# Kernel optimization log

Measured on AMD Instinct MI355X. Metric: run time of the kernel, lower is better.

## Reference

```python
import jax, jax.numpy as jnp
import numpy as np

E = 300000        # num_edges
T = 3000000       # num_triplets
D = 128           # edge_message_dim
N_RAD = 6
N_SPH = 7
D_DOWN = 64       # edge_down_dim
D_BAS = 8         # basis_embed_dim


def _w(key, fan_in, fan_out):
    return jax.random.normal(key, (fan_in, fan_out), jnp.float32) / np.sqrt(fan_in)


def setup_inputs() -> dict:
    key = jax.random.key(0)
    ks = jax.random.split(key, 32)
    inp = {
        "x": jax.random.normal(ks[0], (E, D), jnp.float32),
        "rbf": jax.random.uniform(ks[1], (E, N_RAD), jnp.float32),
        "sbf": jax.random.uniform(ks[2], (T, N_SPH * N_RAD), jnp.float32),
        "idx_kj": jax.random.randint(ks[3], (T,), 0, E),
        "idx_ji": jax.random.randint(ks[4], (T,), 0, E),
        # basis projections (bias-free)
        "w_rbf1": _w(ks[5], N_RAD, D_BAS),
        "w_rbf2": _w(ks[6], D_BAS, D),
        "w_sbf1": _w(ks[7], N_SPH * N_RAD, D_BAS),
        "w_sbf2": _w(ks[8], D_BAS, D_DOWN),
        # message linears (with bias)
        "w_kj": _w(ks[9], D, D), "b_kj": jnp.zeros((D,), jnp.float32),
        "w_ji": _w(ks[10], D, D), "b_ji": jnp.zeros((D,), jnp.float32),
        # down / up projections (bias-free)
        "w_down": _w(ks[11], D, D_DOWN),
        "w_up": _w(ks[12], D_DOWN, D),
        # residual block before skip + dense
        "res1_w1": _w(ks[13], D, D), "res1_b1": jnp.zeros((D,), jnp.float32),
        "res1_w2": _w(ks[14], D, D), "res1_b2": jnp.zeros((D,), jnp.float32),
        "w_bs": _w(ks[15], D, D), "b_bs": jnp.zeros((D,), jnp.float32),
        # two residual blocks after skip
        "res2_w1": _w(ks[16], D, D), "res2_b1": jnp.zeros((D,), jnp.float32),
        "res2_w2": _w(ks[17], D, D), "res2_b2": jnp.zeros((D,), jnp.float32),
        "res3_w1": _w(ks[18], D, D), "res3_b1": jnp.zeros((D,), jnp.float32),
        "res3_w2": _w(ks[19], D, D), "res3_b2": jnp.zeros((D,), jnp.float32),
    }
    return inp


def _res_block(h, w1, b1, w2, b2):
    # h + act(lin2(act(lin1(h)))) with Swish(beta=1) == silu
    return h + jax.nn.silu(jax.nn.silu(h @ w1 + b1) @ w2 + b2)


def reference(x, rbf, sbf, idx_kj, idx_ji,
              w_rbf1, w_rbf2, w_sbf1, w_sbf2,
              w_kj, b_kj, w_ji, b_ji, w_down, w_up,
              res1_w1, res1_b1, res1_w2, res1_b2, w_bs, b_bs,
              res2_w1, res2_b1, res2_w2, res2_b2,
              res3_w1, res3_b1, res3_w2, res3_b2):
    act = jax.nn.silu
    x_ji = act(x @ w_ji + b_ji)                       # [E, D]
    x_kj = act(x @ w_kj + b_kj)                       # [E, D]
    rbf_e = (rbf @ w_rbf1) @ w_rbf2                   # [E, D]
    x_kj = act((x_kj * rbf_e) @ w_down)               # [E, D_DOWN]
    sbf_e = (sbf @ w_sbf1) @ w_sbf2                   # [T, D_DOWN]
    m = x_kj[idx_kj] * sbf_e                          # gather + Hadamard [T, D_DOWN]
    agg = jax.ops.segment_sum(m, idx_ji, num_segments=x.shape[0])  # [E, D_DOWN]
    x_kj = act(agg @ w_up)                            # [E, D]
    h = _res_block(x_ji + x_kj, res1_w1, res1_b1, res1_w2, res1_b2)
    h = act(h @ w_bs + b_bs) + x                      # skip connection
    h = _res_block(h, res2_w1, res2_b1, res2_w2, res2_b2)
    h = _res_block(h, res3_w1, res3_b1, res3_w2, res3_b2)
    return h
```

## Files before the change

kernel.cpp:

```cpp
#include <hip/hip_runtime.h>
#include <hip/hip_bf16.h>


typedef __attribute__((ext_vector_type(8))) short bf16x8;
typedef __attribute__((ext_vector_type(4))) float f32x4;
typedef __attribute__((ext_vector_type(4))) unsigned int u32x4;

__device__ __forceinline__ float silu_f(float v) {
    return v * __builtin_amdgcn_rcpf(1.0f + __expf(-v));
}
__device__ __forceinline__ short f2bf(float f) {
    unsigned u = __float_as_uint(f);
    unsigned r = u + 0x7fffu + ((u >> 16) & 1u);
    return (short)(r >> 16);
}
__device__ __forceinline__ float bf2f(short s) {
    return __uint_as_float(((unsigned)(unsigned short)s) << 16);
}

__device__ __forceinline__ unsigned cvt_pk_bf16(float a, float b) {
    __hip_bfloat162 h = __float22bfloat162_rn(float2{a, b});
    return *reinterpret_cast<unsigned*>(&h);
}
__device__ __forceinline__ void split44(f32x4 a, f32x4 b, bf16x8& hi, bf16x8& lo) {
    float f[8] = {a[0], a[1], a[2], a[3], b[0], b[1], b[2], b[3]};
    u32x4 H, L;
    #pragma unroll
    for (int j = 0; j < 4; ++j) {
        const float f0 = f[2 * j], f1 = f[2 * j + 1];
        const unsigned h = cvt_pk_bf16(f0, f1);
        const float r0 = f0 - __uint_as_float(h << 16);
        const float r1 = f1 - __uint_as_float(h & 0xffff0000u);
        H[j] = h;
        L[j] = cvt_pk_bf16(r0, r1);
    }
    hi = __builtin_bit_cast(bf16x8, H);
    lo = __builtin_bit_cast(bf16x8, L);
}

__device__ __forceinline__ void gll16(const void* g, void* l) {
    __builtin_amdgcn_global_load_lds((const __attribute__((address_space(1))) void*)g,
                                     (__attribute__((address_space(3))) void*)l, 16, 0, 0);
}
__device__ __forceinline__ void stage16(const char* g, short* l, int lane, int wid) {
    #pragma unroll
    for (int i = 0; i < 4; ++i) {
        const int off = ((i * 4 + wid) << 10);
        gll16(g + off + lane * 16, (char*)l + off);
    }
}
__device__ __forceinline__ void stage8(const char* g, short* l, int lane, int wid) {
    #pragma unroll
    for (int i = 0; i < 2; ++i) {
        const int off = ((i * 4 + wid) << 10);
        gll16(g + off + lane * 16, (char*)l + off);
    }
}

template<int NF>
__device__ __forceinline__ void mfma_ks(bf16x8 ah, bf16x8 al, const short* slot,
                                        int acol, int kq, f32x4* acc) {
    #pragma unroll
    for (int n = 0; n < NF; ++n) {
        const int c = n * 16 + acol;
        const int x = (c >> 2) & 1;
        const int sw = (kq ^ (c & 3)) << 3;
        const bf16x8 bh = *(const bf16x8*)&slot[c * 64 + x * 32 + sw];
        const bf16x8 bl = *(const bf16x8*)&slot[c * 64 + (x ^ 1) * 32 + sw];
        acc[n] = __builtin_amdgcn_mfma_f32_16x16x32_bf16(ah, bh, acc[n], 0, 0, 0);
        acc[n] = __builtin_amdgcn_mfma_f32_16x16x32_bf16(al, bh, acc[n], 0, 0, 0);
        acc[n] = __builtin_amdgcn_mfma_f32_16x16x32_bf16(ah, bl, acc[n], 0, 0, 0);
    }
}
template<int NF>
__device__ __forceinline__ void gphase(f32x4 a0, f32x4 a1, const short* slot,
                                       int acol, int kq, f32x4* acc) {
    bf16x8 ah, al; split44(a0, a1, ah, al);
    mfma_ks<NF>(ah, al, slot, acol, kq, acc);
}
template<int NF>
__device__ __forceinline__ void tphase(const float* tl, int rowbase, int q,
                                       int kq, int acol, const short* slot, f32x4* acc) {
    const f32x4 ta = *(const f32x4*)&tl[rowbase + q * 32 + kq * 8];
    const f32x4 tb = *(const f32x4*)&tl[rowbase + q * 32 + kq * 8 + 4];
    bf16x8 ah, al; split44(ta, tb, ah, al);
    mfma_ks<NF>(ah, al, slot, acol, kq, acc);
}

__device__ __forceinline__ void tgemm4(const char* img, const char* imgnext,
                                       short* sA, short* sB, const float* tl, int rb,
                                       int kq, int acol, int lane, int wid, f32x4* acc)
{
    stage16(img + 16384, sB, lane, wid);
    tphase<8>(tl, rb, 0, kq, acol, sA, acc); __syncthreads();
    stage16(img + 32768, sA, lane, wid);
    tphase<8>(tl, rb, 1, kq, acol, sB, acc); __syncthreads();
    stage16(img + 49152, sB, lane, wid);
    tphase<8>(tl, rb, 2, kq, acol, sA, acc); __syncthreads();
    if (imgnext) stage16(imgnext, sA, lane, wid);
    tphase<8>(tl, rb, 3, kq, acol, sB, acc); __syncthreads();
}

#define TPITCH 132

struct WDesc { const float* src; char* dst; int K; int N; };
struct WPrepArgs { WDesc w[11]; };

__global__ void wprep_kernel(WPrepArgs args) {
    const WDesc d = args.w[blockIdx.y];
    const int h = blockIdx.x;
    if (h * 32 >= d.K) return;
    char* slab = d.dst + (size_t)h * d.N * 128;
    for (int idx = threadIdx.x; idx < d.N * 4; idx += 256) {
        const int c = idx >> 2, ch = idx & 3;
        bf16x8 hi, lo;
        #pragma unroll
        for (int j = 0; j < 8; ++j) {
            const float f = d.src[(size_t)(h * 32 + ch * 8 + j) * d.N + c];
            const short hb = f2bf(f);
            hi[j] = hb;
            lo[j] = f2bf(f - bf2f(hb));
        }
        const int x = (c >> 2) & 1;
        const int sw = (ch ^ (c & 3)) * 16;
        *(bf16x8*)(slab + c * 128 + x * 64 + sw)       = hi;
        *(bf16x8*)(slab + c * 128 + (x ^ 1) * 64 + sw) = lo;
    }
}


__global__ void rbf1_kernel(const float* __restrict__ rbf, const float* __restrict__ w_rbf1,
                            float* __restrict__ re1, int E) {
    const int i = blockIdx.x * 256 + threadIdx.x;
    const int e = i >> 3, p = i & 7;
    if (e < E) {
        float s = 0.f;
        #pragma unroll
        for (int q = 0; q < 6; ++q) s = fmaf(rbf[e * 6 + q], w_rbf1[q * 8 + p], s);
        re1[i] = s;
    }
}

__global__ void count_rank_kernel(const int* __restrict__ idx_ji, int* __restrict__ cnt,
                                  int* __restrict__ rank, int T) {
    const int i = (blockIdx.x * 256 + threadIdx.x) * 4;
    if (i + 3 < T) {
        const int4 j = *(const int4*)&idx_ji[i];
        int4 r;
        r.x = atomicAdd(&cnt[j.x], 1);
        r.y = atomicAdd(&cnt[j.y], 1);
        r.z = atomicAdd(&cnt[j.z], 1);
        r.w = atomicAdd(&cnt[j.w], 1);
        *(int4*)&rank[i] = r;
    } else {
        for (int k = i; k < T; ++k) rank[k] = atomicAdd(&cnt[idx_ji[k]], 1);
    }
}

__global__ void scan_partial_kernel(const int* __restrict__ cnt, int* __restrict__ partial, int E) {
    __shared__ int red[256];
    const int tid = threadIdx.x;
    const int base = blockIdx.x * 1024 + tid * 4;
    int s = 0;
    #pragma unroll
    for (int i = 0; i < 4; ++i) { const int g = base + i; if (g < E) s += cnt[g]; }
    red[tid] = s;
    __syncthreads();
    for (int off = 128; off > 0; off >>= 1) {
        if (tid < off) red[tid] += red[tid + off];
        __syncthreads();
    }
    if (tid == 0) partial[blockIdx.x] = red[0];
}

__global__ void scan_block_kernel(const int* __restrict__ partial, int* __restrict__ blockoff,
                                  int NB, int* offsets, int E) {
    __shared__ int red[256];
    const int tid = threadIdx.x;
    int v[4]; int s = 0;
    #pragma unroll
    for (int i = 0; i < 4; ++i) { const int g = tid * 4 + i; v[i] = (g < NB) ? partial[g] : 0; s += v[i]; }
    red[tid] = s;
    __syncthreads();
    for (int off = 1; off < 256; off <<= 1) {
        const int add = (tid >= off) ? red[tid - off] : 0;
        __syncthreads();
        red[tid] += add;
        __syncthreads();
    }
    int excl = (tid == 0) ? 0 : red[tid - 1];
    #pragma unroll
    for (int i = 0; i < 4; ++i) { const int g = tid * 4 + i; if (g < NB) blockoff[g] = excl; excl += v[i]; }
    if (tid == 255) offsets[E] = red[255];
}

__global__ void scan_final_kernel(const int* __restrict__ cnt, const int* __restrict__ blockoff,
                                  int* __restrict__ offsets, int E) {
    __shared__ int red[256];
    const int tid = threadIdx.x;
    const int base = blockIdx.x * 1024 + tid * 4;
    int v[4]; int s = 0;
    #pragma unroll
    for (int i = 0; i < 4; ++i) { const int g = base + i; v[i] = (g < E) ? cnt[g] : 0; s += v[i]; }
    red[tid] = s;
    __syncthreads();
    for (int off = 1; off < 256; off <<= 1) {
        const int add = (tid >= off) ? red[tid - off] : 0;
        __syncthreads();
        red[tid] += add;
        __syncthreads();
    }
    int run = blockoff[blockIdx.x] + ((tid == 0) ? 0 : red[tid - 1]);
    #pragma unroll
    for (int i = 0; i < 4; ++i) {
        const int g = base + i;
        if (g < E) offsets[g] = run;
        run += v[i];
    }
}

__launch_bounds__(256, 3)
__global__ void e1fill_kernel(const float* __restrict__ sbf, const float* __restrict__ w_sbf1,
                              const int* __restrict__ idx_ji, const int* __restrict__ idx_kj,
                              const int* __restrict__ rank, const int* __restrict__ offsets,
                              float* __restrict__ E1p, int* __restrict__ kjp, int T)
{
    __shared__ float s_lds[256 * 43];
    const int tid = threadIdx.x;
    const long long t0 = (long long)blockIdx.x * 256;
    const int nrow = min(256, (int)(T - t0));
    const int nel  = nrow * 42;
    const float* base = sbf + t0 * 42;

    for (int i = tid * 4; i + 3 < nel; i += 1024) {
        const float4 v = *(const float4*)&base[i];
        s_lds[(i + 0) + (i + 0) / 42] = v.x;
        s_lds[(i + 1) + (i + 1) / 42] = v.y;
        s_lds[(i + 2) + (i + 2) / 42] = v.z;
        s_lds[(i + 3) + (i + 3) / 42] = v.w;
    }
    const int tail0 = nel & ~3;
    if (tid < nel - tail0) { const int g = tail0 + tid; s_lds[g + g / 42] = base[g]; }
    __syncthreads();

    const int t = (int)t0 + tid;
    if (t >= T) return;
    const float* srow = &s_lds[tid * 43];
    float e1[8] = {0.f, 0.f, 0.f, 0.f, 0.f, 0.f, 0.f, 0.f};
    #pragma unroll
    for (int q = 0; q < 42; ++q) {
        const float s = srow[q];
        #pragma unroll
        for (int p = 0; p < 8; ++p) e1[p] = fmaf(s, w_sbf1[q * 8 + p], e1[p]);
    }
    const int ji  = idx_ji[t];
    const int pos = offsets[ji] + rank[t];
    *(float4*)&E1p[(size_t)pos * 8]     = *(float4*)&e1[0];
    *(float4*)&E1p[(size_t)pos * 8 + 4] = *(float4*)&e1[4];
    kjp[pos] = idx_kj[t];
}

__launch_bounds__(256, 4)
__global__ void gather_kernel(const float* __restrict__ E1p, const int* __restrict__ kjp,
                              const float* __restrict__ w_sbf2, const int* __restrict__ offsets,
                              const float* __restrict__ xkjd, float* __restrict__ agg, int E)
{
    const int tid  = threadIdx.x;
    const int lane = tid & 63;
    const int e    = blockIdx.x * 4 + (tid >> 6);

    float w2[8];
    #pragma unroll
    for (int p = 0; p < 8; ++p) w2[p] = w_sbf2[p * 64 + lane];

    if (e >= E) return;
    const int j0 = __builtin_amdgcn_readfirstlane(offsets[e]);
    const int j1 = __builtin_amdgcn_readfirstlane(offsets[e + 1]);

    float acc = 0.f;
    if (j0 < j1) {
        int kj = __builtin_amdgcn_readfirstlane(kjp[j0]);
        float4 ea = *(const float4*)&E1p[(size_t)j0 * 8];
        float4 eb = *(const float4*)&E1p[(size_t)j0 * 8 + 4];
        for (int j = j0; j < j1; ++j) {
            const float xv = xkjd[(size_t)kj * 64 + lane];
            int kn = 0; float4 ean = {}, ebn = {};
            if (j + 1 < j1) {
                kn  = __builtin_amdgcn_readfirstlane(kjp[j + 1]);
                ean = *(const float4*)&E1p[(size_t)(j + 1) * 8];
                ebn = *(const float4*)&E1p[(size_t)(j + 1) * 8 + 4];
            }
            float sv = ea.x * w2[0];
            sv = fmaf(ea.y, w2[1], sv);
            sv = fmaf(ea.z, w2[2], sv);
            sv = fmaf(ea.w, w2[3], sv);
            sv = fmaf(eb.x, w2[4], sv);
            sv = fmaf(eb.y, w2[5], sv);
            sv = fmaf(eb.z, w2[6], sv);
            sv = fmaf(eb.w, w2[7], sv);
            acc = fmaf(xv, sv, acc);
            kj = kn; ea = ean; eb = ebn;
        }
    }
    agg[(size_t)e * 64 + lane] = acc;
}

__launch_bounds__(256, 2)
__global__ void k1_kernel(const float* __restrict__ x, const char* __restrict__ wkj_i,
                          const float* __restrict__ b_kj, const float* __restrict__ re1,
                          const float* __restrict__ w_rbf2, const char* __restrict__ wdn_i,
                          float* __restrict__ W3, int E)
{
    __shared__ short slotA[8192], slotB[8192];
    __shared__ float t_lds[64 * TPITCH];
    __shared__ float w2_lds[8 * 128];
    const int tid = threadIdx.x, lane = tid & 63, wid = tid >> 6;
    const int acol = lane & 15, kq = lane >> 4;
    const int rowW = blockIdx.x * 64 + wid * 16;
    const int arow = rowW + acol;
    const bool av = arow < E;

    stage16(wkj_i, slotA, lane, wid);
    const float* xr = x + (size_t)arow * 128;
    f32x4 a[4][2];
    #pragma unroll
    for (int ks = 0; ks < 4; ++ks) {
        a[ks][0] = f32x4{0.f, 0.f, 0.f, 0.f}; a[ks][1] = f32x4{0.f, 0.f, 0.f, 0.f};
        if (av) { a[ks][0] = *(const f32x4*)&xr[ks * 32 + kq * 8];
                  a[ks][1] = *(const f32x4*)&xr[ks * 32 + kq * 8 + 4]; }
    }
    float bv[8];
    #pragma unroll
    for (int n = 0; n < 8; ++n) bv[n] = b_kj[n * 16 + acol];
    f32x4 e1a[4], e1b[4];
    #pragma unroll
    for (int r = 0; r < 4; ++r) {
        const int ge = rowW + kq * 4 + r;
        e1a[r] = f32x4{0.f, 0.f, 0.f, 0.f}; e1b[r] = f32x4{0.f, 0.f, 0.f, 0.f};
        if (ge < E) { e1a[r] = *(const f32x4*)&re1[(size_t)ge * 8];
                      e1b[r] = *(const f32x4*)&re1[(size_t)ge * 8 + 4]; }
    }
    for (int i = tid; i < 1024; i += 256) w2_lds[i] = w_rbf2[i];
    __syncthreads();

    f32x4 acc[8];
    #pragma unroll
    for (int n = 0; n < 8; ++n) acc[n] = f32x4{0.f, 0.f, 0.f, 0.f};

    stage16(wkj_i + 16384, slotB, lane, wid);
    gphase<8>(a[0][0], a[0][1], slotA, acol, kq, acc); __syncthreads();
    stage16(wkj_i + 32768, slotA, lane, wid);
    gphase<8>(a[1][0], a[1][1], slotB, acol, kq, acc); __syncthreads();
    stage16(wkj_i + 49152, slotB, lane, wid);
    gphase<8>(a[2][0], a[2][1], slotA, acol, kq, acc); __syncthreads();
    stage8(wdn_i, slotA, lane, wid);
    gphase<8>(a[3][0], a[3][1], slotB, acol, kq, acc); __syncthreads();

    #pragma unroll
    for (int n = 0; n < 8; ++n) {
        const int c = n * 16 + acol;
        float w2c[8];
        #pragma unroll
        for (int p = 0; p < 8; ++p) w2c[p] = w2_lds[p * 128 + c];
        #pragma unroll
        for (int r = 0; r < 4; ++r) {
            float s = e1a[r][0] * w2c[0];
            s = fmaf(e1a[r][1], w2c[1], s);
            s = fmaf(e1a[r][2], w2c[2], s);
            s = fmaf(e1a[r][3], w2c[3], s);
            s = fmaf(e1b[r][0], w2c[4], s);
            s = fmaf(e1b[r][1], w2c[5], s);
            s = fmaf(e1b[r][2], w2c[6], s);
            s = fmaf(e1b[r][3], w2c[7], s);
            t_lds[(wid * 16 + kq * 4 + r) * TPITCH + c] = silu_f(acc[n][r] + bv[n]) * s;
        }
    }
    __syncthreads();

    f32x4 acc2[4];
    #pragma unroll
    for (int n = 0; n < 4; ++n) acc2[n] = f32x4{0.f, 0.f, 0.f, 0.f};
    const int rb = (wid * 16 + acol) * TPITCH;

    stage8(wdn_i + 8192, slotB, lane, wid);
    tphase<4>(t_lds, rb, 0, kq, acol, slotA, acc2); __syncthreads();
    stage8(wdn_i + 16384, slotA, lane, wid);
    tphase<4>(t_lds, rb, 1, kq, acol, slotB, acc2); __syncthreads();
    stage8(wdn_i + 24576, slotB, lane, wid);
    tphase<4>(t_lds, rb, 2, kq, acol, slotA, acc2); __syncthreads();
    tphase<4>(t_lds, rb, 3, kq, acol, slotB, acc2);

    #pragma unroll
    for (int n = 0; n < 4; ++n) {
        const int c = n * 16 + acol;
        #pragma unroll
        for (int r = 0; r < 4; ++r) {
            const int ge = rowW + kq * 4 + r;
            if (ge < E) W3[(size_t)ge * 64 + c] = silu_f(acc2[n][r]);
        }
    }
}

struct KBigArgs {
    const float* x; const float* W4; float* out;
    const char *wji, *wup, *r1w1, *r1w2, *wbs, *r2w1, *r2w2, *r3w1, *r3w2;
    const float *bji, *r1b1, *r1b2, *bbs, *r2b1, *r2b2, *r3b1, *r3b2;
    int E;
};

__launch_bounds__(256, 2)
__global__ void kbig_kernel(KBigArgs A_)
{
    __shared__ short slotA[8192], slotB[8192];
    __shared__ float t_lds[64 * TPITCH];
    const int tid = threadIdx.x, lane = tid & 63, wid = tid >> 6;
    const int acol = lane & 15, kq = lane >> 4;
    const int rowW = blockIdx.x * 64 + wid * 16;
    const int arow = rowW + acol;
    const int E = A_.E;
    const bool av = arow < E;
    const int rb = (wid * 16 + acol) * TPITCH;

    stage16(A_.wji, slotA, lane, wid);

    const float* xr = A_.x + (size_t)arow * 128;
    const float* wr = A_.W4 + (size_t)arow * 64;
    f32x4 a[4][2], u[2][2];
    #pragma unroll
    for (int ks = 0; ks < 4; ++ks) {
        a[ks][0] = f32x4{0.f, 0.f, 0.f, 0.f}; a[ks][1] = f32x4{0.f, 0.f, 0.f, 0.f};
        if (av) { a[ks][0] = *(const f32x4*)&xr[ks * 32 + kq * 8];
                  a[ks][1] = *(const f32x4*)&xr[ks * 32 + kq * 8 + 4]; }
    }
    #pragma unroll
    for (int ks = 0; ks < 2; ++ks) {
        u[ks][0] = f32x4{0.f, 0.f, 0.f, 0.f}; u[ks][1] = f32x4{0.f, 0.f, 0.f, 0.f};
        if (av) { u[ks][0] = *(const f32x4*)&wr[ks * 32 + kq * 8];
                  u[ks][1] = *(const f32x4*)&wr[ks * 32 + kq * 8 + 4]; }
    }
    __syncthreads();

    f32x4 acc[8];
    #pragma unroll
    for (int n = 0; n < 8; ++n) acc[n] = f32x4{0.f, 0.f, 0.f, 0.f};

    stage16(A_.wji + 16384, slotB, lane, wid);
    gphase<8>(a[0][0], a[0][1], slotA, acol, kq, acc); __syncthreads();
    stage16(A_.wji + 32768, slotA, lane, wid);
    gphase<8>(a[1][0], a[1][1], slotB, acol, kq, acc); __syncthreads();
    stage16(A_.wji + 49152, slotB, lane, wid);
    gphase<8>(a[2][0], a[2][1], slotA, acol, kq, acc); __syncthreads();
    stage16(A_.wup, slotA, lane, wid);
    gphase<8>(a[3][0], a[3][1], slotB, acol, kq, acc); __syncthreads();

    float res[8][4];
    #pragma unroll
    for (int n = 0; n < 8; ++n) {
        const float bv = A_.bji[n * 16 + acol];
        #pragma unroll
        for (int r = 0; r < 4; ++r) { res[n][r] = silu_f(acc[n][r] + bv); acc[n][r] = 0.f; }
    }

    stage16(A_.wup + 16384, slotB, lane, wid);
    gphase<8>(u[0][0], u[0][1], slotA, acol, kq, acc); __syncthreads();
    stage16(A_.r1w1, slotA, lane, wid);
    gphase<8>(u[1][0], u[1][1], slotB, acol, kq, acc); __syncthreads();

    #pragma unroll
    for (int n = 0; n < 8; ++n) {
        const int c = n * 16 + acol;
        #pragma unroll
        for (int r = 0; r < 4; ++r) {
            res[n][r] += silu_f(acc[n][r]);
            t_lds[(wid * 16 + kq * 4 + r) * TPITCH + c] = res[n][r];
            acc[n][r] = 0.f;
        }
    }
    __syncthreads();

    tgemm4(A_.r1w1, A_.r1w2, slotA, slotB, t_lds, rb, kq, acol, lane, wid, acc);
    #pragma unroll
    for (int n = 0; n < 8; ++n) {
        const float bv = A_.r1b1[n * 16 + acol];
        const int c = n * 16 + acol;
        #pragma unroll
        for (int r = 0; r < 4; ++r) {
            t_lds[(wid * 16 + kq * 4 + r) * TPITCH + c] = silu_f(acc[n][r] + bv);
            acc[n][r] = 0.f;
        }
    }
    __syncthreads();

    tgemm4(A_.r1w2, A_.wbs, slotA, slotB, t_lds, rb, kq, acol, lane, wid, acc);
    #pragma unroll
    for (int n = 0; n < 8; ++n) {
        const float bv = A_.r1b2[n * 16 + acol];
        const int c = n * 16 + acol;
        #pragma unroll
        for (int r = 0; r < 4; ++r) {
            t_lds[(wid * 16 + kq * 4 + r) * TPITCH + c] = res[n][r] + silu_f(acc[n][r] + bv);
            acc[n][r] = 0.f;
        }
    }
    __syncthreads();

    tgemm4(A_.wbs, A_.r2w1, slotA, slotB, t_lds, rb, kq, acol, lane, wid, acc);
    #pragma unroll
    for (int n = 0; n < 8; ++n) {
        const float bv = A_.bbs[n * 16 + acol];
        const int c = n * 16 + acol;
        #pragma unroll
        for (int r = 0; r < 4; ++r) {
            const int ge = rowW + kq * 4 + r;
            const float xv = (ge < E) ? A_.x[(size_t)ge * 128 + c] : 0.f;
            res[n][r] = silu_f(acc[n][r] + bv) + xv;
            t_lds[(wid * 16 + kq * 4 + r) * TPITCH + c] = res[n][r];
            acc[n][r] = 0.f;
        }
    }
    __syncthreads();

    tgemm4(A_.r2w1, A_.r2w2, slotA, slotB, t_lds, rb, kq, acol, lane, wid, acc);
    #pragma unroll
    for (int n = 0; n < 8; ++n) {
        const float bv = A_.r2b1[n * 16 + acol];
        const int c = n * 16 + acol;
        #pragma unroll
        for (int r = 0; r < 4; ++r) {
            t_lds[(wid * 16 + kq * 4 + r) * TPITCH + c] = silu_f(acc[n][r] + bv);
            acc[n][r] = 0.f;
        }
    }
    __syncthreads();

    tgemm4(A_.r2w2, A_.r3w1, slotA, slotB, t_lds, rb, kq, acol, lane, wid, acc);
    #pragma unroll
    for (int n = 0; n < 8; ++n) {
        const float bv = A_.r2b2[n * 16 + acol];
        const int c = n * 16 + acol;
        #pragma unroll
        for (int r = 0; r < 4; ++r) {
            res[n][r] += silu_f(acc[n][r] + bv);
            t_lds[(wid * 16 + kq * 4 + r) * TPITCH + c] = res[n][r];
            acc[n][r] = 0.f;
        }
    }
    __syncthreads();

    tgemm4(A_.r3w1, A_.r3w2, slotA, slotB, t_lds, rb, kq, acol, lane, wid, acc);
    #pragma unroll
    for (int n = 0; n < 8; ++n) {
        const float bv = A_.r3b1[n * 16 + acol];
        const int c = n * 16 + acol;
        #pragma unroll
        for (int r = 0; r < 4; ++r) {
            t_lds[(wid * 16 + kq * 4 + r) * TPITCH + c] = silu_f(acc[n][r] + bv);
            acc[n][r] = 0.f;
        }
    }
    __syncthreads();

    tgemm4(A_.r3w2, nullptr, slotA, slotB, t_lds, rb, kq, acol, lane, wid, acc);
    #pragma unroll
    for (int n = 0; n < 8; ++n) {
        const float bv = A_.r3b2[n * 16 + acol];
        const int c = n * 16 + acol;
        #pragma unroll
        for (int r = 0; r < 4; ++r) {
            const int ge = rowW + kq * 4 + r;
            if (ge < E)
                A_.out[(size_t)ge * 128 + c] = res[n][r] + silu_f(acc[n][r] + bv);
        }
    }
}


extern "C" void kernel_launch(void* const* d_in, const int* in_sizes, int n_in,
                              void* d_out, int out_size, void* d_ws, size_t ws_size,
                              hipStream_t stream)
{
    const float* x      = (const float*)d_in[0];
    const float* rbf    = (const float*)d_in[1];
    const float* sbf    = (const float*)d_in[2];
    const int*   idx_kj = (const int*)d_in[3];
    const int*   idx_ji = (const int*)d_in[4];
    const float* w_rbf1 = (const float*)d_in[5];
    const float* w_rbf2 = (const float*)d_in[6];
    const float* w_sbf1 = (const float*)d_in[7];
    const float* w_sbf2 = (const float*)d_in[8];
    const float* w_kj   = (const float*)d_in[9];
    const float* b_kj   = (const float*)d_in[10];
    const float* w_ji   = (const float*)d_in[11];
    const float* b_ji   = (const float*)d_in[12];
    const float* w_down = (const float*)d_in[13];
    const float* w_up   = (const float*)d_in[14];
    const float* r1w1   = (const float*)d_in[15];
    const float* r1b1   = (const float*)d_in[16];
    const float* r1w2   = (const float*)d_in[17];
    const float* r1b2   = (const float*)d_in[18];
    const float* w_bs   = (const float*)d_in[19];
    const float* b_bs   = (const float*)d_in[20];
    const float* r2w1   = (const float*)d_in[21];
    const float* r2b1   = (const float*)d_in[22];
    const float* r2w2   = (const float*)d_in[23];
    const float* r2b2   = (const float*)d_in[24];
    const float* r3w1   = (const float*)d_in[25];
    const float* r3b1   = (const float*)d_in[26];
    const float* r3w2   = (const float*)d_in[27];
    const float* r3b2   = (const float*)d_in[28];

    const int E = in_sizes[0] / 128;
    const int T = in_sizes[2] / 42;

    float* OUT = (float*)d_out;
    float* W3  = (float*)((char*)d_ws + (size_t)E * 128 * 4);
    float* W4  = (float*)((char*)d_ws + (size_t)E * 128 * 4
                                      + (size_t)E * 64 * 4);

    int*   cnt      = (int*)d_ws;
    int*   offsets  = cnt + (E + 64);
    int*   partial  = offsets + (E + 64);
    int*   blockoff = partial + 1024;
    float* E1p      = (float*)((char*)d_ws + (4u << 20));
    int*   kjp      = (int*)((char*)d_ws + (102u << 20));
    float* re1      = (float*)((char*)d_ws + (116u << 20));
    char*  wimg     = (char*)d_ws + (130u << 20);
    int*   rank     = (int*)((char*)d_ws + (134u << 20));

    char* wkj_i  = wimg;
    char* wji_i  = wimg + 65536;
    char* wdn_i  = wimg + 131072;
    char* wup_i  = wimg + 163840;
    char* r1w1_i = wimg + 196608;
    char* r1w2_i = wimg + 262144;
    char* wbs_i  = wimg + 327680;
    char* r2w1_i = wimg + 393216;
    char* r2w2_i = wimg + 458752;
    char* r3w1_i = wimg + 524288;
    char* r3w2_i = wimg + 589824;

    WPrepArgs pa;
    pa.w[0]  = {w_kj,   wkj_i,  128, 128};
    pa.w[1]  = {w_ji,   wji_i,  128, 128};
    pa.w[2]  = {w_down, wdn_i,  128,  64};
    pa.w[3]  = {w_up,   wup_i,   64, 128};
    pa.w[4]  = {r1w1,   r1w1_i, 128, 128};
    pa.w[5]  = {r1w2,   r1w2_i, 128, 128};
    pa.w[6]  = {w_bs,   wbs_i,  128, 128};
    pa.w[7]  = {r2w1,   r2w1_i, 128, 128};
    pa.w[8]  = {r2w2,   r2w2_i, 128, 128};
    pa.w[9]  = {r3w1,   r3w1_i, 128, 128};
    pa.w[10] = {r3w2,   r3w2_i, 128, 128};

    const dim3 b256(256);
    const int gB  = (E + 63) / 64;
    const int gT  = (T + 255) / 256;
    const int gT4 = (T + 1023) / 1024;
    const int NB  = (E + 1023) / 1024;
    const int gE4 = (E + 3) / 4;
    const int gR  = (E * 8 + 255) / 256;

    wprep_kernel<<<dim3(4, 11), b256, 0, stream>>>(pa);
    rbf1_kernel<<<gR, b256, 0, stream>>>(rbf, w_rbf1, re1, E);
    hipMemsetAsync(cnt, 0, (size_t)E * 4, stream);
    count_rank_kernel<<<gT4, b256, 0, stream>>>(idx_ji, cnt, rank, T);
    scan_partial_kernel<<<NB, b256, 0, stream>>>(cnt, partial, E);
    scan_block_kernel<<<1, b256, 0, stream>>>(partial, blockoff, NB, offsets, E);
    scan_final_kernel<<<NB, b256, 0, stream>>>(cnt, blockoff, offsets, E);
    e1fill_kernel<<<gT, b256, 0, stream>>>(sbf, w_sbf1, idx_ji, idx_kj, rank, offsets, E1p, kjp, T);

    k1_kernel<<<gB, b256, 0, stream>>>(x, wkj_i, b_kj, re1, w_rbf2, wdn_i, W3, E);
    gather_kernel<<<gE4, b256, 0, stream>>>(E1p, kjp, w_sbf2, offsets, W3, W4, E);

    KBigArgs ka;
    ka.x = x; ka.W4 = W4; ka.out = OUT;
    ka.wji = wji_i; ka.wup = wup_i; ka.r1w1 = r1w1_i; ka.r1w2 = r1w2_i; ka.wbs = wbs_i;
    ka.r2w1 = r2w1_i; ka.r2w2 = r2w2_i; ka.r3w1 = r3w1_i; ka.r3w2 = r3w2_i;
    ka.bji = b_ji; ka.r1b1 = r1b1; ka.r1b2 = r1b2; ka.bbs = b_bs;
    ka.r2b1 = r2b1; ka.r2b2 = r2b2; ka.r3b1 = r3b1; ka.r3b2 = r3b2;
    ka.E = E;
    kbig_kernel<<<gB, b256, 0, stream>>>(ka);
}
```

Measured before the change: 1.199 ms.

## Give each wave two 16-row tiles so LDS weight fragments are reused

```diff
diff --git a/kernel.cpp b/kernel.cpp
--- a/kernel.cpp
+++ b/kernel.cpp
@@ -44,22 +44,23 @@
 }
 __device__ __forceinline__ void stage16(const char* g, short* l, int lane, int wid) {
     #pragma unroll
+    for (int i = 0; i < 8; ++i) {
+        const int off = ((i * 2 + wid) << 10);
+        gll16(g + off + lane * 16, (char*)l + off);
+    }
+}
+__device__ __forceinline__ void stage8(const char* g, short* l, int lane, int wid) {
+    #pragma unroll
     for (int i = 0; i < 4; ++i) {
-        const int off = ((i * 4 + wid) << 10);
+        const int off = ((i * 2 + wid) << 10);
         gll16(g + off + lane * 16, (char*)l + off);
     }
 }
-__device__ __forceinline__ void stage8(const char* g, short* l, int lane, int wid) {
-    #pragma unroll
-    for (int i = 0; i < 2; ++i) {
-        const int off = ((i * 4 + wid) << 10);
-        gll16(g + off + lane * 16, (char*)l + off);
-    }
-}
 
 template<int NF>
-__device__ __forceinline__ void mfma_ks(bf16x8 ah, bf16x8 al, const short* slot,
-                                        int acol, int kq, f32x4* acc) {
+__device__ __forceinline__ void mfma_ks2(bf16x8 ah0, bf16x8 al0, bf16x8 ah1, bf16x8 al1,
+                                         const short* slot, int acol, int kq,
+                                         f32x4* acc0, f32x4* acc1) {
     #pragma unroll
     for (int n = 0; n < NF; ++n) {
         const int c = n * 16 + acol;
@@ -67,38 +68,50 @@
         const int sw = (kq ^ (c & 3)) << 3;
         const bf16x8 bh = *(const bf16x8*)&slot[c * 64 + x * 32 + sw];
         const bf16x8 bl = *(const bf16x8*)&slot[c * 64 + (x ^ 1) * 32 + sw];
-        acc[n] = __builtin_amdgcn_mfma_f32_16x16x32_bf16(ah, bh, acc[n], 0, 0, 0);
-        acc[n] = __builtin_amdgcn_mfma_f32_16x16x32_bf16(al, bh, acc[n], 0, 0, 0);
-        acc[n] = __builtin_amdgcn_mfma_f32_16x16x32_bf16(ah, bl, acc[n], 0, 0, 0);
+        acc0[n] = __builtin_amdgcn_mfma_f32_16x16x32_bf16(ah0, bh, acc0[n], 0, 0, 0);
+        acc0[n] = __builtin_amdgcn_mfma_f32_16x16x32_bf16(al0, bh, acc0[n], 0, 0, 0);
+        acc0[n] = __builtin_amdgcn_mfma_f32_16x16x32_bf16(ah0, bl, acc0[n], 0, 0, 0);
+        acc1[n] = __builtin_amdgcn_mfma_f32_16x16x32_bf16(ah1, bh, acc1[n], 0, 0, 0);
+        acc1[n] = __builtin_amdgcn_mfma_f32_16x16x32_bf16(al1, bh, acc1[n], 0, 0, 0);
+        acc1[n] = __builtin_amdgcn_mfma_f32_16x16x32_bf16(ah1, bl, acc1[n], 0, 0, 0);
     }
 }
 template<int NF>
-__device__ __forceinline__ void gphase(f32x4 a0, f32x4 a1, const short* slot,
-                                       int acol, int kq, f32x4* acc) {
-    bf16x8 ah, al; split44(a0, a1, ah, al);
-    mfma_ks<NF>(ah, al, slot, acol, kq, acc);
+__device__ __forceinline__ void gphase2(f32x4 a00, f32x4 a01, f32x4 a10, f32x4 a11,
+                                        const short* slot, int acol, int kq,
+                                        f32x4* acc0, f32x4* acc1) {
+    bf16x8 ah0, al0, ah1, al1;
+    split44(a00, a01, ah0, al0);
+    split44(a10, a11, ah1, al1);
+    mfma_ks2<NF>(ah0, al0, ah1, al1, slot, acol, kq, acc0, acc1);
 }
 template<int NF>
-__device__ __forceinline__ void tphase(const float* tl, int rowbase, int q,
-                                       int kq, int acol, const short* slot, f32x4* acc) {
-    const f32x4 ta = *(const f32x4*)&tl[rowbase + q * 32 + kq * 8];
-    const f32x4 tb = *(const f32x4*)&tl[rowbase + q * 32 + kq * 8 + 4];
-    bf16x8 ah, al; split44(ta, tb, ah, al);
-    mfma_ks<NF>(ah, al, slot, acol, kq, acc);
+__device__ __forceinline__ void tphase2(const float* tl, int rb0, int rb1, int q,
+                                        int kq, int acol, const short* slot,
+                                        f32x4* acc0, f32x4* acc1) {
+    const f32x4 ta0 = *(const f32x4*)&tl[rb0 + q * 32 + kq * 8];
+    const f32x4 tb0 = *(const f32x4*)&tl[rb0 + q * 32 + kq * 8 + 4];
+    const f32x4 ta1 = *(const f32x4*)&tl[rb1 + q * 32 + kq * 8];
+    const f32x4 tb1 = *(const f32x4*)&tl[rb1 + q * 32 + kq * 8 + 4];
+    bf16x8 ah0, al0, ah1, al1;
+    split44(ta0, tb0, ah0, al0);
+    split44(ta1, tb1, ah1, al1);
+    mfma_ks2<NF>(ah0, al0, ah1, al1, slot, acol, kq, acc0, acc1);
 }
 
 __device__ __forceinline__ void tgemm4(const char* img, const char* imgnext,
-                                       short* sA, short* sB, const float* tl, int rb,
-                                       int kq, int acol, int lane, int wid, f32x4* acc)
+                                       short* sA, short* sB, const float* tl,
+                                       int rb0, int rb1, int kq, int acol,
+                                       int lane, int wid, f32x4* acc0, f32x4* acc1)
 {
     stage16(img + 16384, sB, lane, wid);
-    tphase<8>(tl, rb, 0, kq, acol, sA, acc); __syncthreads();
+    tphase2<8>(tl, rb0, rb1, 0, kq, acol, sA, acc0, acc1); __syncthreads();
     stage16(img + 32768, sA, lane, wid);
-    tphase<8>(tl, rb, 1, kq, acol, sB, acc); __syncthreads();
+    tphase2<8>(tl, rb0, rb1, 1, kq, acol, sB, acc0, acc1); __syncthreads();
     stage16(img + 49152, sB, lane, wid);
-    tphase<8>(tl, rb, 2, kq, acol, sA, acc); __syncthreads();
+    tphase2<8>(tl, rb0, rb1, 2, kq, acol, sA, acc0, acc1); __syncthreads();
     if (imgnext) stage16(imgnext, sA, lane, wid);
-    tphase<8>(tl, rb, 3, kq, acol, sB, acc); __syncthreads();
+    tphase2<8>(tl, rb0, rb1, 3, kq, acol, sB, acc0, acc1); __syncthreads();
 }
 
 #define TPITCH 132
@@ -305,7 +318,7 @@
     agg[(size_t)e * 64 + lane] = acc;
 }
 
-__launch_bounds__(256, 2)
+__launch_bounds__(128, 1)
 __global__ void k1_kernel(const float* __restrict__ x, const char* __restrict__ wkj_i,
                           const float* __restrict__ b_kj, const float* __restrict__ re1,
                           const float* __restrict__ w_rbf2, const char* __restrict__ wdn_i,
@@ -316,87 +329,102 @@
     __shared__ float w2_lds[8 * 128];
     const int tid = threadIdx.x, lane = tid & 63, wid = tid >> 6;
     const int acol = lane & 15, kq = lane >> 4;
-    const int rowW = blockIdx.x * 64 + wid * 16;
-    const int arow = rowW + acol;
-    const bool av = arow < E;
+    const int row0 = blockIdx.x * 64 + wid * 32;
 
     stage16(wkj_i, slotA, lane, wid);
-    const float* xr = x + (size_t)arow * 128;
-    f32x4 a[4][2];
-    #pragma unroll
-    for (int ks = 0; ks < 4; ++ks) {
-        a[ks][0] = f32x4{0.f, 0.f, 0.f, 0.f}; a[ks][1] = f32x4{0.f, 0.f, 0.f, 0.f};
-        if (av) { a[ks][0] = *(const f32x4*)&xr[ks * 32 + kq * 8];
-                  a[ks][1] = *(const f32x4*)&xr[ks * 32 + kq * 8 + 4]; }
+
+    f32x4 a[2][4][2];
+    #pragma unroll
+    for (int rf = 0; rf < 2; ++rf) {
+        const int ar = row0 + rf * 16 + acol;
+        const bool av = ar < E;
+        const float* xr = x + (size_t)ar * 128;
+        #pragma unroll
+        for (int ks = 0; ks < 4; ++ks) {
+            a[rf][ks][0] = f32x4{0.f, 0.f, 0.f, 0.f}; a[rf][ks][1] = f32x4{0.f, 0.f, 0.f, 0.f};
+            if (av) { a[rf][ks][0] = *(const f32x4*)&xr[ks * 32 + kq * 8];
+                      a[rf][ks][1] = *(const f32x4*)&xr[ks * 32 + kq * 8 + 4]; }
+        }
     }
     float bv[8];
     #pragma unroll
     for (int n = 0; n < 8; ++n) bv[n] = b_kj[n * 16 + acol];
-    f32x4 e1a[4], e1b[4];
-    #pragma unroll
-    for (int r = 0; r < 4; ++r) {
-        const int ge = rowW + kq * 4 + r;
-        e1a[r] = f32x4{0.f, 0.f, 0.f, 0.f}; e1b[r] = f32x4{0.f, 0.f, 0.f, 0.f};
-        if (ge < E) { e1a[r] = *(const f32x4*)&re1[(size_t)ge * 8];
-                      e1b[r] = *(const f32x4*)&re1[(size_t)ge * 8 + 4]; }
-    }
-    for (int i = tid; i < 1024; i += 256) w2_lds[i] = w_rbf2[i];
-    __syncthreads();
-
-    f32x4 acc[8];
-    #pragma unroll
-    for (int n = 0; n < 8; ++n) acc[n] = f32x4{0.f, 0.f, 0.f, 0.f};
+    f32x4 e1a[2][4], e1b[2][4];
+    #pragma unroll
+    for (int rf = 0; rf < 2; ++rf)
+        #pragma unroll
+        for (int r = 0; r < 4; ++r) {
+            const int ge = row0 + rf * 16 + kq * 4 + r;
+            e1a[rf][r] = f32x4{0.f, 0.f, 0.f, 0.f}; e1b[rf][r] = f32x4{0.f, 0.f, 0.f, 0.f};
+            if (ge < E) { e1a[rf][r] = *(const f32x4*)&re1[(size_t)ge * 8];
+                          e1b[rf][r] = *(const f32x4*)&re1[(size_t)ge * 8 + 4]; }
+        }
+    for (int i = tid; i < 1024; i += 128) w2_lds[i] = w_rbf2[i];
+    __syncthreads();
+
+    f32x4 acc0[8], acc1[8];
+    #pragma unroll
+    for (int n = 0; n < 8; ++n) { acc0[n] = f32x4{0.f, 0.f, 0.f, 0.f}; acc1[n] = f32x4{0.f, 0.f, 0.f, 0.f}; }
 
     stage16(wkj_i + 16384, slotB, lane, wid);
-    gphase<8>(a[0][0], a[0][1], slotA, acol, kq, acc); __syncthreads();
+    gphase2<8>(a[0][0][0], a[0][0][1], a[1][0][0], a[1][0][1], slotA, acol, kq, acc0, acc1); __syncthreads();
     stage16(wkj_i + 32768, slotA, lane, wid);
-    gphase<8>(a[1][0], a[1][1], slotB, acol, kq, acc); __syncthreads();
+    gphase2<8>(a[0][1][0], a[0][1][1], a[1][1][0], a[1][1][1], slotB, acol, kq, acc0, acc1); __syncthreads();
     stage16(wkj_i + 49152, slotB, lane, wid);
-    gphase<8>(a[2][0], a[2][1], slotA, acol, kq, acc); __syncthreads();
+    gphase2<8>(a[0][2][0], a[0][2][1], a[1][2][0], a[1][2][1], slotA, acol, kq, acc0, acc1); __syncthreads();
     stage8(wdn_i, slotA, lane, wid);
-    gphase<8>(a[3][0], a[3][1], slotB, acol, kq, acc); __syncthreads();
-
-    #pragma unroll
-    for (int n = 0; n < 8; ++n) {
-        const int c = n * 16 + acol;
-        float w2c[8];
-        #pragma unroll
-        for (int p = 0; p < 8; ++p) w2c[p] = w2_lds[p * 128 + c];
-        #pragma unroll
-        for (int r = 0; r < 4; ++r) {
-            float s = e1a[r][0] * w2c[0];
-            s = fmaf(e1a[r][1], w2c[1], s);
-            s = fmaf(e1a[r][2], w2c[2], s);
-            s = fmaf(e1a[r][3], w2c[3], s);
-            s = fmaf(e1b[r][0], w2c[4], s);
-            s = fmaf(e1b[r][1], w2c[5], s);
-            s = fmaf(e1b[r][2], w2c[6], s);
-            s = fmaf(e1b[r][3], w2c[7], s);
-            t_lds[(wid * 16 + kq * 4 + r) * TPITCH + c] = silu_f(acc[n][r] + bv[n]) * s;
-        }
-    }
-    __syncthreads();
-
-    f32x4 acc2[4];
-    #pragma unroll
-    for (int n = 0; n < 4; ++n) acc2[n] = f32x4{0.f, 0.f, 0.f, 0.f};
-    const int rb = (wid * 16 + acol) * TPITCH;
+    gphase2<8>(a[0][3][0], a[0][3][1], a[1][3][0], a[1][3][1], slotB, acol, kq, acc0, acc1); __syncthreads();
+
+    #pragma unroll
+    for (int rf = 0; rf < 2; ++rf) {
+        f32x4* acc = rf ? acc1 : acc0;
+        #pragma unroll
+        for (int n = 0; n < 8; ++n) {
+            const int c = n * 16 + acol;
+            float w2c[8];
+            #pragma unroll
+            for (int p = 0; p < 8; ++p) w2c[p] = w2_lds[p * 128 + c];
+            #pragma unroll
+            for (int r = 0; r < 4; ++r) {
+                float s = e1a[rf][r][0] * w2c[0];
+                s = fmaf(e1a[rf][r][1], w2c[1], s);
+                s = fmaf(e1a[rf][r][2], w2c[2], s);
+                s = fmaf(e1a[rf][r][3], w2c[3], s);
+                s = fmaf(e1b[rf][r][0], w2c[4], s);
+                s = fmaf(e1b[rf][r][1], w2c[5], s);
+                s = fmaf(e1b[rf][r][2], w2c[6], s);
+                s = fmaf(e1b[rf][r][3], w2c[7], s);
+                t_lds[(wid * 32 + rf * 16 + kq * 4 + r) * TPITCH + c] = silu_f(acc[n][r] + bv[n]) * s;
+            }
+        }
+    }
+    __syncthreads();
+
+    f32x4 acc20[4], acc21[4];
+    #pragma unroll
+    for (int n = 0; n < 4; ++n) { acc20[n] = f32x4{0.f, 0.f, 0.f, 0.f}; acc21[n] = f32x4{0.f, 0.f, 0.f, 0.f}; }
+    const int rb0 = (wid * 32 + acol) * TPITCH;
+    const int rb1 = (wid * 32 + 16 + acol) * TPITCH;
 
     stage8(wdn_i + 8192, slotB, lane, wid);
-    tphase<4>(t_lds, rb, 0, kq, acol, slotA, acc2); __syncthreads();
+    tphase2<4>(t_lds, rb0, rb1, 0, kq, acol, slotA, acc20, acc21); __syncthreads();
     stage8(wdn_i + 16384, slotA, lane, wid);
-    tphase<4>(t_lds, rb, 1, kq, acol, slotB, acc2); __syncthreads();
+    tphase2<4>(t_lds, rb0, rb1, 1, kq, acol, slotB, acc20, acc21); __syncthreads();
     stage8(wdn_i + 24576, slotB, lane, wid);
-    tphase<4>(t_lds, rb, 2, kq, acol, slotA, acc2); __syncthreads();
-    tphase<4>(t_lds, rb, 3, kq, acol, slotB, acc2);
-
-    #pragma unroll
-    for (int n = 0; n < 4; ++n) {
-        const int c = n * 16 + acol;
-        #pragma unroll
-        for (int r = 0; r < 4; ++r) {
-            const int ge = rowW + kq * 4 + r;
-            if (ge < E) W3[(size_t)ge * 64 + c] = silu_f(acc2[n][r]);
+    tphase2<4>(t_lds, rb0, rb1, 2, kq, acol, slotA, acc20, acc21); __syncthreads();
+    tphase2<4>(t_lds, rb0, rb1, 3, kq, acol, slotB, acc20, acc21);
+
+    #pragma unroll
+    for (int rf = 0; rf < 2; ++rf) {
+        f32x4* acc = rf ? acc21 : acc20;
+        #pragma unroll
+        for (int n = 0; n < 4; ++n) {
+            const int c = n * 16 + acol;
+            #pragma unroll
+            for (int r = 0; r < 4; ++r) {
+                const int ge = row0 + rf * 16 + kq * 4 + r;
+                if (ge < E) W3[(size_t)ge * 64 + c] = silu_f(acc[n][r]);
+            }
         }
     }
 }
@@ -408,168 +436,208 @@
     int E;
 };
 
-__launch_bounds__(256, 2)
+__launch_bounds__(128, 1)
 __global__ void kbig_kernel(KBigArgs A_)
 {
     __shared__ short slotA[8192], slotB[8192];
     __shared__ float t_lds[64 * TPITCH];
     const int tid = threadIdx.x, lane = tid & 63, wid = tid >> 6;
     const int acol = lane & 15, kq = lane >> 4;
-    const int rowW = blockIdx.x * 64 + wid * 16;
-    const int arow = rowW + acol;
+    const int row0 = blockIdx.x * 64 + wid * 32;
     const int E = A_.E;
-    const bool av = arow < E;
-    const int rb = (wid * 16 + acol) * TPITCH;
+    const int rb0 = (wid * 32 + acol) * TPITCH;
+    const int rb1 = (wid * 32 + 16 + acol) * TPITCH;
 
     stage16(A_.wji, slotA, lane, wid);
 
-    const float* xr = A_.x + (size_t)arow * 128;
-    const float* wr = A_.W4 + (size_t)arow * 64;
-    f32x4 a[4][2], u[2][2];
-    #pragma unroll
-    for (int ks = 0; ks < 4; ++ks) {
-        a[ks][0] = f32x4{0.f, 0.f, 0.f, 0.f}; a[ks][1] = f32x4{0.f, 0.f, 0.f, 0.f};
-        if (av) { a[ks][0] = *(const f32x4*)&xr[ks * 32 + kq * 8];
-                  a[ks][1] = *(const f32x4*)&xr[ks * 32 + kq * 8 + 4]; }
-    }
-    #pragma unroll
-    for (int ks = 0; ks < 2; ++ks) {
-        u[ks][0] = f32x4{0.f, 0.f, 0.f, 0.f}; u[ks][1] = f32x4{0.f, 0.f, 0.f, 0.f};
-        if (av) { u[ks][0] = *(const f32x4*)&wr[ks * 32 + kq * 8];
-                  u[ks][1] = *(const f32x4*)&wr[ks * 32 + kq * 8 + 4]; }
-    }
-    __syncthreads();
-
-    f32x4 acc[8];
-    #pragma unroll
-    for (int n = 0; n < 8; ++n) acc[n] = f32x4{0.f, 0.f, 0.f, 0.f};
+    f32x4 a[2][4][2], u[2][2][2];
+    #pragma unroll
+    for (int rf = 0; rf < 2; ++rf) {
+        const int ar = row0 + rf * 16 + acol;
+        const bool av = ar < E;
+        const float* xr = A_.x + (size_t)ar * 128;
+        const float* wr = A_.W4 + (size_t)ar * 64;
+        #pragma unroll
+        for (int ks = 0; ks < 4; ++ks) {
+            a[rf][ks][0] = f32x4{0.f, 0.f, 0.f, 0.f}; a[rf][ks][1] = f32x4{0.f, 0.f, 0.f, 0.f};
+            if (av) { a[rf][ks][0] = *(const f32x4*)&xr[ks * 32 + kq * 8];
+                      a[rf][ks][1] = *(const f32x4*)&xr[ks * 32 + kq * 8 + 4]; }
+        }
+        #pragma unroll
+        for (int ks = 0; ks < 2; ++ks) {
+            u[rf][ks][0] = f32x4{0.f, 0.f, 0.f, 0.f}; u[rf][ks][1] = f32x4{0.f, 0.f, 0.f, 0.f};
+            if (av) { u[rf][ks][0] = *(const f32x4*)&wr[ks * 32 + kq * 8];
+                      u[rf][ks][1] = *(const f32x4*)&wr[ks * 32 + kq * 8 + 4]; }
+        }
+    }
+    __syncthreads();
+
+    f32x4 acc0[8], acc1[8];
+    #pragma unroll
+    for (int n = 0; n < 8; ++n) { acc0[n] = f32x4{0.f, 0.f, 0.f, 0.f}; acc1[n] = f32x4{0.f, 0.f, 0.f, 0.f}; }
 
     stage16(A_.wji + 16384, slotB, lane, wid);
-    gphase<8>(a[0][0], a[0][1], slotA, acol, kq, acc); __syncthreads();
+    gphase2<8>(a[0][0][0], a[0][0][1], a[1][0][0], a[1][0][1], slotA, acol, kq, acc0, acc1); __syncthreads();
     stage16(A_.wji + 32768, slotA, lane, wid);
-    gphase<8>(a[1][0], a[1][1], slotB, acol, kq, acc); __syncthreads();
+    gphase2<8>(a[0][1][0], a[0][1][1], a[1][1][0], a[1][1][1], slotB, acol, kq, acc0, acc1); __syncthreads();
     stage16(A_.wji + 49152, slotB, lane, wid);
-    gphase<8>(a[2][0], a[2][1], slotA, acol, kq, acc); __syncthreads();
+    gphase2<8>(a[0][2][0], a[0][2][1], a[1][2][0], a[1][2][1], slotA, acol, kq, acc0, acc1); __syncthreads();
     stage16(A_.wup, slotA, lane, wid);
-    gphase<8>(a[3][0], a[3][1], slotB, acol, kq, acc); __syncthreads();
-
-    float res[8][4];
-    #pragma unroll
-    for (int n = 0; n < 8; ++n) {
-        const float bv = A_.bji[n * 16 + acol];
-        #pragma unroll
-        for (int r = 0; r < 4; ++r) { res[n][r] = silu_f(acc[n][r] + bv); acc[n][r] = 0.f; }
+    gphase2<8>(a[0][3][0], a[0][3][1], a[1][3][0], a[1][3][1], slotB, acol, kq, acc0, acc1); __syncthreads();
+
+    float res[2][8][4];
+    #pragma unroll
+    for (int rf = 0; rf < 2; ++rf) {
+        f32x4* acc = rf ? acc1 : acc0;
+        #pragma unroll
+        for (int n = 0; n < 8; ++n) {
+            const float bv = A_.bji[n * 16 + acol];
+            #pragma unroll
+            for (int r = 0; r < 4; ++r) { res[rf][n][r] = silu_f(acc[n][r] + bv); acc[n][r] = 0.f; }
+        }
     }
 
     stage16(A_.wup + 16384, slotB, lane, wid);
-    gphase<8>(u[0][0], u[0][1], slotA, acol, kq, acc); __syncthreads();
+    gphase2<8>(u[0][0][0], u[0][0][1], u[1][0][0], u[1][0][1], slotA, acol, kq, acc0, acc1); __syncthreads();
     stage16(A_.r1w1, slotA, lane, wid);
-    gphase<8>(u[1][0], u[1][1], slotB, acol, kq, acc); __syncthreads();
-
-    #pragma unroll
-    for (int n = 0; n < 8; ++n) {
-        const int c = n * 16 + acol;
-        #pragma unroll
-        for (int r = 0; r < 4; ++r) {
-            res[n][r] += silu_f(acc[n][r]);
-            t_lds[(wid * 16 + kq * 4 + r) * TPITCH + c] = res[n][r];
-            acc[n][r] = 0.f;
-        }
-    }
-    __syncthreads();
-
-    tgemm4(A_.r1w1, A_.r1w2, slotA, slotB, t_lds, rb, kq, acol, lane, wid, acc);
-    #pragma unroll
-    for (int n = 0; n < 8; ++n) {
-        const float bv = A_.r1b1[n * 16 + acol];
-        const int c = n * 16 + acol;
-        #pragma unroll
-        for (int r = 0; r < 4; ++r) {
-            t_lds[(wid * 16 + kq * 4 + r) * TPITCH + c] = silu_f(acc[n][r] + bv);
-            acc[n][r] = 0.f;
-        }
-    }
-    __syncthreads();
-
-    tgemm4(A_.r1w2, A_.wbs, slotA, slotB, t_lds, rb, kq, acol, lane, wid, acc);
-    #pragma unroll
-    for (int n = 0; n < 8; ++n) {
-        const float bv = A_.r1b2[n * 16 + acol];
-        const int c = n * 16 + acol;
-        #pragma unroll
-        for (int r = 0; r < 4; ++r) {
-            t_lds[(wid * 16 + kq * 4 + r) * TPITCH + c] = res[n][r] + silu_f(acc[n][r] + bv);
-            acc[n][r] = 0.f;
-        }
-    }
-    __syncthreads();
-
-    tgemm4(A_.wbs, A_.r2w1, slotA, slotB, t_lds, rb, kq, acol, lane, wid, acc);
-    #pragma unroll
-    for (int n = 0; n < 8; ++n) {
-        const float bv = A_.bbs[n * 16 + acol];
-        const int c = n * 16 + acol;
-        #pragma unroll
-        for (int r = 0; r < 4; ++r) {
-            const int ge = rowW + kq * 4 + r;
-            const float xv = (ge < E) ? A_.x[(size_t)ge * 128 + c] : 0.f;
-            res[n][r] = silu_f(acc[n][r] + bv) + xv;
-            t_lds[(wid * 16 + kq * 4 + r) * TPITCH + c] = res[n][r];
-            acc[n][r] = 0.f;
-        }
-    }
-    __syncthreads();
-
-    tgemm4(A_.r2w1, A_.r2w2, slotA, slotB, t_lds, rb, kq, acol, lane, wid, acc);
-    #pragma unroll
-    for (int n = 0; n < 8; ++n) {
-        const float bv = A_.r2b1[n * 16 + acol];
-        const int c = n * 16 + acol;
-        #pragma unroll
-        for (int r = 0; r < 4; ++r) {
-            t_lds[(wid * 16 + kq * 4 + r) * TPITCH + c] = silu_f(acc[n][r] + bv);
-            acc[n][r] = 0.f;
-        }
-    }
-    __syncthreads();
-
-    tgemm4(A_.r2w2, A_.r3w1, slotA, slotB, t_lds, rb, kq, acol, lane, wid, acc);
-    #pragma unroll
-    for (int n = 0; n < 8; ++n) {
-        const float bv = A_.r2b2[n * 16 + acol];
-        const int c = n * 16 + acol;
-        #pragma unroll
-        for (int r = 0; r < 4; ++r) {
-            res[n][r] += silu_f(acc[n][r] + bv);
-            t_lds[(wid * 16 + kq * 4 + r) * TPITCH + c] = res[n][r];
-            acc[n][r] = 0.f;
-        }
-    }
-    __syncthreads();
-
-    tgemm4(A_.r3w1, A_.r3w2, slotA, slotB, t_lds, rb, kq, acol, lane, wid, acc);
-    #pragma unroll
-    for (int n = 0; n < 8; ++n) {
-        const float bv = A_.r3b1[n * 16 + acol];
-        const int c = n * 16 + acol;
-        #pragma unroll
-        for (int r = 0; r < 4; ++r) {
-            t_lds[(wid * 16 + kq * 4 + r) * TPITCH + c] = silu_f(acc[n][r] + bv);
-            acc[n][r] = 0.f;
-        }
-    }
-    __syncthreads();
-
-    tgemm4(A_.r3w2, nullptr, slotA, slotB, t_lds, rb, kq, acol, lane, wid, acc);
-    #pragma unroll
-    for (int n = 0; n < 8; ++n) {
-        const float bv = A_.r3b2[n * 16 + acol];
-        const int c = n * 16 + acol;
-        #pragma unroll
-        for (int r = 0; r < 4; ++r) {
-            const int ge = rowW + kq * 4 + r;
-            if (ge < E)
-                A_.out[(size_t)ge * 128 + c] = res[n][r] + silu_f(acc[n][r] + bv);
+    gphase2<8>(u[0][1][0], u[0][1][1], u[1][1][0], u[1][1][1], slotB, acol, kq, acc0, acc1); __syncthreads();
+
+    #pragma unroll
+    for (int rf = 0; rf < 2; ++rf) {
+        f32x4* acc = rf ? acc1 : acc0;
+        #pragma unroll
+        for (int n = 0; n < 8; ++n) {
+            const int c = n * 16 + acol;
+            #pragma unroll
+            for (int r = 0; r < 4; ++r) {
+                res[rf][n][r] += silu_f(acc[n][r]);
+                t_lds[(wid * 32 + rf * 16 + kq * 4 + r) * TPITCH + c] = res[rf][n][r];
+                acc[n][r] = 0.f;
+            }
+        }
+    }
+    __syncthreads();
+
+    tgemm4(A_.r1w1, A_.r1w2, slotA, slotB, t_lds, rb0, rb1, kq, acol, lane, wid, acc0, acc1);
+    #pragma unroll
+    for (int rf = 0; rf < 2; ++rf) {
+        f32x4* acc = rf ? acc1 : acc0;
+        #pragma unroll
+        for (int n = 0; n < 8; ++n) {
+            const float bv = A_.r1b1[n * 16 + acol];
+            const int c = n * 16 + acol;
+            #pragma unroll
+            for (int r = 0; r < 4; ++r) {
+                t_lds[(wid * 32 + rf * 16 + kq * 4 + r) * TPITCH + c] = silu_f(acc[n][r] + bv);
+                acc[n][r] = 0.f;
+            }
+        }
+    }
+    __syncthreads();
+
+    tgemm4(A_.r1w2, A_.wbs, slotA, slotB, t_lds, rb0, rb1, kq, acol, lane, wid, acc0, acc1);
+    #pragma unroll
+    for (int rf = 0; rf < 2; ++rf) {
+        f32x4* acc = rf ? acc1 : acc0;
+        #pragma unroll
+        for (int n = 0; n < 8; ++n) {
+            const float bv = A_.r1b2[n * 16 + acol];
+            const int c = n * 16 + acol;
+            #pragma unroll
+            for (int r = 0; r < 4; ++r) {
+                t_lds[(wid * 32 + rf * 16 + kq * 4 + r) * TPITCH + c] = res[rf][n][r] + silu_f(acc[n][r] + bv);
+                acc[n][r] = 0.f;
+            }
+        }
+    }
+    __syncthreads();
+
+    tgemm4(A_.wbs, A_.r2w1, slotA, slotB, t_lds, rb0, rb1, kq, acol, lane, wid, acc0, acc1);
+    #pragma unroll
+    for (int rf = 0; rf < 2; ++rf) {
+        f32x4* acc = rf ? acc1 : acc0;
+        #pragma unroll
+        for (int n = 0; n < 8; ++n) {
+            const float bv = A_.bbs[n * 16 + acol];
+            const int c = n * 16 + acol;
+            #pragma unroll
+            for (int r = 0; r < 4; ++r) {
+                const int ge = row0 + rf * 16 + kq * 4 + r;
+                const float xv = (ge < E) ? A_.x[(size_t)ge * 128 + c] : 0.f;
+                res[rf][n][r] = silu_f(acc[n][r] + bv) + xv;
+                t_lds[(wid * 32 + rf * 16 + kq * 4 + r) * TPITCH + c] = res[rf][n][r];
+                acc[n][r] = 0.f;
+            }
+        }
+    }
+    __syncthreads();
+
+    tgemm4(A_.r2w1, A_.r2w2, slotA, slotB, t_lds, rb0, rb1, kq, acol, lane, wid, acc0, acc1);
+    #pragma unroll
+    for (int rf = 0; rf < 2; ++rf) {
+        f32x4* acc = rf ? acc1 : acc0;
+        #pragma unroll
+        for (int n = 0; n < 8; ++n) {
+            const float bv = A_.r2b1[n * 16 + acol];
+            const int c = n * 16 + acol;
+            #pragma unroll
+            for (int r = 0; r < 4; ++r) {
+                t_lds[(wid * 32 + rf * 16 + kq * 4 + r) * TPITCH + c] = silu_f(acc[n][r] + bv);
+                acc[n][r] = 0.f;
+            }
+        }
+    }
+    __syncthreads();
+
+    tgemm4(A_.r2w2, A_.r3w1, slotA, slotB, t_lds, rb0, rb1, kq, acol, lane, wid, acc0, acc1);
+    #pragma unroll
+    for (int rf = 0; rf < 2; ++rf) {
+        f32x4* acc = rf ? acc1 : acc0;
+        #pragma unroll
+        for (int n = 0; n < 8; ++n) {
+            const float bv = A_.r2b2[n * 16 + acol];
+            const int c = n * 16 + acol;
+            #pragma unroll
+            for (int r = 0; r < 4; ++r) {
+                res[rf][n][r] += silu_f(acc[n][r] + bv);
+                t_lds[(wid * 32 + rf * 16 + kq * 4 + r) * TPITCH + c] = res[rf][n][r];
+                acc[n][r] = 0.f;
+            }
+        }
+    }
+    __syncthreads();
+
+    tgemm4(A_.r3w1, A_.r3w2, slotA, slotB, t_lds, rb0, rb1, kq, acol, lane, wid, acc0, acc1);
+    #pragma unroll
+    for (int rf = 0; rf < 2; ++rf) {
+        f32x4* acc = rf ? acc1 : acc0;
+        #pragma unroll
+        for (int n = 0; n < 8; ++n) {
+            const float bv = A_.r3b1[n * 16 + acol];
+            const int c = n * 16 + acol;
+            #pragma unroll
+            for (int r = 0; r < 4; ++r) {
+                t_lds[(wid * 32 + rf * 16 + kq * 4 + r) * TPITCH + c] = silu_f(acc[n][r] + bv);
+                acc[n][r] = 0.f;
+            }
+        }
+    }
+    __syncthreads();
+
+    tgemm4(A_.r3w2, nullptr, slotA, slotB, t_lds, rb0, rb1, kq, acol, lane, wid, acc0, acc1);
+    #pragma unroll
+    for (int rf = 0; rf < 2; ++rf) {
+        f32x4* acc = rf ? acc1 : acc0;
+        #pragma unroll
+        for (int n = 0; n < 8; ++n) {
+            const float bv = A_.r3b2[n * 16 + acol];
+            const int c = n * 16 + acol;
+            #pragma unroll
+            for (int r = 0; r < 4; ++r) {
+                const int ge = row0 + rf * 16 + kq * 4 + r;
+                if (ge < E)
+                    A_.out[(size_t)ge * 128 + c] = res[rf][n][r] + silu_f(acc[n][r] + bv);
+            }
         }
     }
 }
@@ -652,7 +720,7 @@
     pa.w[9]  = {r3w1,   r3w1_i, 128, 128};
     pa.w[10] = {r3w2,   r3w2_i, 128, 128};
 
-    const dim3 b256(256);
+    const dim3 b256(256), b128(128);
     const int gB  = (E + 63) / 64;
     const int gT  = (T + 255) / 256;
     const int gT4 = (T + 1023) / 1024;
@@ -669,7 +737,7 @@
     scan_final_kernel<<<NB, b256, 0, stream>>>(cnt, blockoff, offsets, E);
     e1fill_kernel<<<gT, b256, 0, stream>>>(sbf, w_sbf1, idx_ji, idx_kj, rank, offsets, E1p, kjp, T);
 
-    k1_kernel<<<gB, b256, 0, stream>>>(x, wkj_i, b_kj, re1, w_rbf2, wdn_i, W3, E);
+    k1_kernel<<<gB, b128, 0, stream>>>(x, wkj_i, b_kj, re1, w_rbf2, wdn_i, W3, E);
     gather_kernel<<<gE4, b256, 0, stream>>>(E1p, kjp, w_sbf2, offsets, W3, W4, E);
 
     KBigArgs ka;
@@ -679,5 +747,5 @@
     ka.bji = b_ji; ka.r1b1 = r1b1; ka.r1b2 = r1b2; ka.bbs = b_bs;
     ka.r2b1 = r2b1; ka.r2b2 = r2b2; ka.r3b1 = r3b1; ka.r3b2 = r3b2;
     ka.E = E;
-    kbig_kernel<<<gB, b256, 0, stream>>>(ka);
-}
+    kbig_kernel<<<gB, b128, 0, stream>>>(ka);
+}
```

Result: slower. 1.459 ms (+21.6%).
